# Performance work log

Measured on AMD Instinct MI355X. Metric: run time of the kernel, lower is better.

Reference implementation:

```python
import jax, jax.numpy as jnp
import numpy as np

H, C = 4, 32            # heads, per-head out channels -> H*C = 128
NEG = jnp.float32(-1e9) # stand-in for -inf mask (keeps grads finite)
NUM_LOC = 15            # self.num_locations hardcoded to 15


def _tconv(x, src, dst, ea, Wq, bq, Wk, bk, Wv, bv, We, Ws, bs, Wb):
    # PyG TransformerConv(beta=True, concat=True, edge_dim=1)
    N = x.shape[0]
    q = (x @ Wq + bq).reshape(N, H, C)
    k = (x @ Wk + bk).reshape(N, H, C)
    v = (x @ Wv + bv).reshape(N, H, C)
    e = (ea @ We).reshape(-1, H, C)  # edge embedding [E,H,C]
    kj = k[src] + e
    alpha = jnp.einsum('ehc,ehc->eh', q[dst], kj) / jnp.sqrt(jnp.float32(C))
    # scatter-softmax over incoming edges of each dst node
    amax = jax.ops.segment_max(alpha, dst, num_segments=N)
    ex = jnp.exp(alpha - amax[dst])
    den = jax.ops.segment_sum(ex, dst, num_segments=N)
    w = ex / (den[dst] + 1e-16)
    out = jax.ops.segment_sum((v[src] + e) * w[..., None], dst, num_segments=N).reshape(N, H * C)
    xr = x @ Ws + bs  # lin_skip
    beta = jax.nn.sigmoid(jnp.concatenate([out, xr, out - xr], axis=-1) @ Wb)  # [N,1]
    return beta * xr + (1.0 - beta) * out


def _bn(x, g, b):
    # BatchNorm1d in training mode (batch statistics, biased var)
    m = x.mean(0)
    v = ((x - m) ** 2).mean(0)
    return (x - m) * jax.lax.rsqrt(v + 1e-5) * g + b


def _forward_core(fa, edge_index, active_mask):
    (node_type, requests, latency,
     c0_Wq, c0_bq, c0_Wk, c0_bk, c0_Wv, c0_bv, c0_We, c0_Ws, c0_bs, c0_Wb,
     t0_W, t0_b, bn0_g, bn0_b,
     cs_Wq, cs_bq, cs_Wk, cs_bk, cs_Wv, cs_bv, cs_We, cs_Ws, cs_bs, cs_Wb,
     ts_W, ts_b, bns_g, bns_b,
     emb_W1, emb_b1, emb_W2, emb_b2, emb_W3, emb_b3,
     rem_W, rem_b, add_W, add_b) = fa
    src, dst = edge_index[0], edge_index[1]
    ea = latency[:, None]                      # edge_attr [E,1]
    x = jnp.stack([node_type, requests], axis=1)  # [N,2]
    # NetworkGraphEmbeddingConstructor: conv1 + 4 stacked conv/linear/bn blocks
    x = _tconv(x, src, dst, ea, c0_Wq, c0_bq, c0_Wk, c0_bk, c0_Wv, c0_bv, c0_We, c0_Ws, c0_bs, c0_Wb)
    x = _bn(jax.nn.relu(x @ t0_W + t0_b), bn0_g, bn0_b)
    for i in range(4):
        x = _tconv(x, src, dst, ea, cs_Wq[i], cs_bq[i], cs_Wk[i], cs_bk[i], cs_Wv[i], cs_bv[i], cs_We[i], cs_Ws[i], cs_bs[i], cs_Wb[i])
        x = _bn(jax.nn.relu(x @ ts_W[i] + ts_b[i]), bns_g[i], bns_b[i])
    # embedding_transformation MLP
    x = jax.nn.relu(x @ emb_W1 + emb_b1)
    x = jax.nn.relu(x @ emb_W2 + emb_b2)
    x = x @ emb_W3 + emb_b3                    # [N,64]
    # sampling head (batch_index=None branch)
    N = x.shape[0]
    maskf = jnp.where(active_mask == 1, jnp.float32(0.0), NEG)
    loc = jnp.arange(N) < NUM_LOC
    remove_mask = jnp.where(loc, jnp.where(maskf == 0.0, NEG, jnp.float32(0.0)), maskf)
    logits1 = (x @ rem_W + rem_b)[:, 0] + remove_mask
    k1, k2 = jax.random.split(jax.random.key(42))
    a1 = jnp.argmax(logits1 + jax.random.gumbel(k1, (N,), logits1.dtype))  # Categorical sample
    mask2 = maskf.at[a1].set(0.0)
    t = jnp.tanh(x[a1] @ add_W + add_b)        # [64]
    logits2 = x @ t + mask2
    a2 = jnp.argmax(logits2 + jax.random.gumbel(k2, (N,), logits2.dtype))
    log_probs = jnp.stack([jax.nn.log_softmax(logits1)[a1], jax.nn.log_softmax(logits2)[a2]])
    return jnp.stack([logits1, logits2]), jnp.stack([a1, a2]), log_probs


def setup_inputs() -> dict:
    N, E = 50000, 400000
    F, HC, EMB, L = 2, 128, 32, 4
    key = jax.random.key(0)
    kit = iter(jax.random.split(key, 64))
    def w(shape, s=0.1):
        return jax.random.normal(next(kit), shape, jnp.float32) * s
    return {
        'node_type': w((N,), 1.0),
        'requests': jax.random.uniform(next(kit), (N,), jnp.float32),
        'latency': jax.random.uniform(next(kit), (E,), jnp.float32),
        'edge_index': jax.random.randint(next(kit), (2, E), 0, N, jnp.int32),
        'active_mask': jax.random.randint(next(kit), (N,), 0, 2, jnp.int32),
        'c0_Wq': w((F, HC)), 'c0_bq': w((HC,)),
        'c0_Wk': w((F, HC)), 'c0_bk': w((HC,)),
        'c0_Wv': w((F, HC)), 'c0_bv': w((HC,)),
        'c0_We': w((1, HC)),
        'c0_Ws': w((F, HC)), 'c0_bs': w((HC,)),
        'c0_Wb': w((3 * HC, 1)),
        't0_W': w((HC, EMB)), 't0_b': w((EMB,)),
        'bn0_g': jnp.ones((EMB,), jnp.float32), 'bn0_b': jnp.zeros((EMB,), jnp.float32),
        'cs_Wq': w((L, EMB, HC)), 'cs_bq': w((L, HC)),
        'cs_Wk': w((L, EMB, HC)), 'cs_bk': w((L, HC)),
        'cs_Wv': w((L, EMB, HC)), 'cs_bv': w((L, HC)),
        'cs_We': w((L, 1, HC)),
        'cs_Ws': w((L, EMB, HC)), 'cs_bs': w((L, HC)),
        'cs_Wb': w((L, 3 * HC, 1)),
        'ts_W': w((L, HC, EMB)), 'ts_b': w((L, EMB)),
        'bns_g': jnp.ones((L, EMB), jnp.float32), 'bns_b': jnp.zeros((L, EMB), jnp.float32),
        'emb_W1': w((EMB, 128)), 'emb_b1': w((128,)),
        'emb_W2': w((128, 64)), 'emb_b2': w((64,)),
        'emb_W3': w((64, 64)), 'emb_b3': w((64,)),
        'rem_W': w((64, 1)), 'rem_b': w((1,)),
        'add_W': w((64, 64)), 'add_b': w((64,)),
    }


def reference(node_type, requests, latency, edge_index, active_mask,
              c0_Wq, c0_bq, c0_Wk, c0_bk, c0_Wv, c0_bv, c0_We, c0_Ws, c0_bs, c0_Wb,
              t0_W, t0_b, bn0_g, bn0_b,
              cs_Wq, cs_bq, cs_Wk, cs_bk, cs_Wv, cs_bv, cs_We, cs_Ws, cs_bs, cs_Wb,
              ts_W, ts_b, bns_g, bns_b,
              emb_W1, emb_b1, emb_W2, emb_b2, emb_W3, emb_b3,
              rem_W, rem_b, add_W, add_b):
    fa = (node_type, requests, latency,
          c0_Wq, c0_bq, c0_Wk, c0_bk, c0_Wv, c0_bv, c0_We, c0_Ws, c0_bs, c0_Wb,
          t0_W, t0_b, bn0_g, bn0_b,
          cs_Wq, cs_bq, cs_Wk, cs_bk, cs_Wv, cs_bv, cs_We, cs_Ws, cs_bs, cs_Wb,
          ts_W, ts_b, bns_g, bns_b,
          emb_W1, emb_b1, emb_W2, emb_b2, emb_W3, emb_b3,
          rem_W, rem_b, add_W, add_b)
    return _forward_core(fa, edge_index, active_mask)
```

## Files before the change

kernel.cpp:

```cpp
#include <hip/hip_runtime.h>
#include <hip/hip_fp16.h>
#include <cstdint>
#include <math.h>

typedef _Float16 h2 __attribute__((ext_vector_type(2)));

__device__ __forceinline__ h2 f2h2(float a, float b) {
    h2 r; r.x = (_Float16)a; r.y = (_Float16)b; return r;
}
__device__ __forceinline__ float fdot2f(h2 a, h2 b, float c) {
    return __builtin_amdgcn_fdot2(a, b, c, false);
}

union f4h {
    float4 f;
    h2 h[4];
    __half2 u[4];
};

__device__ __forceinline__ uint32_t rotl32(uint32_t x, uint32_t n) {
    return (x << n) | (x >> (32u - n));
}

__device__ __forceinline__ void tf2x32(uint32_t k0, uint32_t k1,
                                       uint32_t x0, uint32_t x1,
                                       uint32_t& o0, uint32_t& o1) {
    uint32_t k2 = k0 ^ k1 ^ 0x1BD11BDAu;
    x0 += k0; x1 += k1;
    x0 += x1; x1 = rotl32(x1, 13); x1 ^= x0;
    x0 += x1; x1 = rotl32(x1, 15); x1 ^= x0;
    x0 += x1; x1 = rotl32(x1, 26); x1 ^= x0;
    x0 += x1; x1 = rotl32(x1, 6);  x1 ^= x0;
    x0 += k1; x1 += k2 + 1u;
    x0 += x1; x1 = rotl32(x1, 17); x1 ^= x0;
    x0 += x1; x1 = rotl32(x1, 29); x1 ^= x0;
    x0 += x1; x1 = rotl32(x1, 16); x1 ^= x0;
    x0 += x1; x1 = rotl32(x1, 24); x1 ^= x0;
    x0 += k2; x1 += k0 + 2u;
    x0 += x1; x1 = rotl32(x1, 13); x1 ^= x0;
    x0 += x1; x1 = rotl32(x1, 15); x1 ^= x0;
    x0 += x1; x1 = rotl32(x1, 26); x1 ^= x0;
    x0 += x1; x1 = rotl32(x1, 6);  x1 ^= x0;
    x0 += k0; x1 += k1 + 3u;
    x0 += x1; x1 = rotl32(x1, 17); x1 ^= x0;
    x0 += x1; x1 = rotl32(x1, 29); x1 ^= x0;
    x0 += x1; x1 = rotl32(x1, 16); x1 ^= x0;
    x0 += x1; x1 = rotl32(x1, 24); x1 ^= x0;
    x0 += k1; x1 += k2 + 4u;
    x0 += x1; x1 = rotl32(x1, 13); x1 ^= x0;
    x0 += x1; x1 = rotl32(x1, 15); x1 ^= x0;
    x0 += x1; x1 = rotl32(x1, 26); x1 ^= x0;
    x0 += x1; x1 = rotl32(x1, 6);  x1 ^= x0;
    x0 += k2; x1 += k0 + 5u;
    o0 = x0; o1 = x1;
}

__device__ float gumbel_at(int n, int which, int N) {
    uint32_t a0, a1, b0, b1;
    tf2x32(0u, 42u, 0u, 2u, a0, a1);
    tf2x32(0u, 42u, 1u, 3u, b0, b1);
    uint32_t gk0 = which ? a1 : a0;
    uint32_t gk1 = which ? b1 : b0;
    int half = N >> 1;
    uint32_t o0, o1, bits;
    if (n < half) { tf2x32(gk0, gk1, (uint32_t)n, (uint32_t)(n + half), o0, o1); bits = o0; }
    else          { tf2x32(gk0, gk1, (uint32_t)(n - half), (uint32_t)n, o0, o1); bits = o1; }
    float f = __uint_as_float((bits >> 9) | 0x3F800000u) - 1.0f;
    float u = fmaxf(1.17549435e-38f, f);
    return -logf(-logf(u));
}

__device__ __forceinline__ uint32_t fmono(float f) {
    uint32_t b = __float_as_uint(f);
    return (b & 0x80000000u) ? ~b : (b | 0x80000000u);
}
__device__ __forceinline__ float funmono(uint32_t u) {
    uint32_t b = (u & 0x80000000u) ? (u & 0x7FFFFFFFu) : ~u;
    return __uint_as_float(b);
}

#define NEGF (-1e9f)
#define ATTNGRID 2048

__global__ void k_hist(const int* __restrict__ dstp, int* __restrict__ deg, int E) {
    int e = blockIdx.x * 256 + threadIdx.x;
    if (e < E) atomicAdd(&deg[dstp[e]], 1);
}

__global__ void k_scan1(const int* __restrict__ deg, int* __restrict__ bsum, int N) {
    __shared__ int s[256];
    int i = blockIdx.x * 256 + threadIdx.x;
    s[threadIdx.x] = (i < N) ? deg[i] : 0;
    __syncthreads();
    for (int st = 128; st > 0; st >>= 1) {
        if (threadIdx.x < st) s[threadIdx.x] += s[threadIdx.x + st];
        __syncthreads();
    }
    if (threadIdx.x == 0) bsum[blockIdx.x] = s[0];
}

__global__ void k_scan2(int* __restrict__ bsum, int nb) {
    __shared__ int s[256];
    int i = threadIdx.x;
    int v = (i < nb) ? bsum[i] : 0;
    s[i] = v;
    __syncthreads();
    for (int st = 1; st < 256; st <<= 1) {
        int t = (i >= st) ? s[i - st] : 0;
        __syncthreads();
        s[i] += t;
        __syncthreads();
    }
    if (i < nb) bsum[i] = s[i] - v;
}

__global__ void k_scan3(const int* __restrict__ deg, const int* __restrict__ bsum,
                        int* __restrict__ rowptr, int* __restrict__ cursor, int N) {
    __shared__ int s[256];
    int i = blockIdx.x * 256 + threadIdx.x;
    int v = (i < N) ? deg[i] : 0;
    s[threadIdx.x] = v;
    __syncthreads();
    for (int st = 1; st < 256; st <<= 1) {
        int t = (threadIdx.x >= st) ? s[threadIdx.x - st] : 0;
        __syncthreads();
        s[threadIdx.x] += t;
        __syncthreads();
    }
    int excl = s[threadIdx.x] - v + bsum[blockIdx.x];
    if (i < N) { rowptr[i] = excl; cursor[i] = excl; }
}

__global__ void k_fill(const int* __restrict__ dstp, const int* __restrict__ srcp,
                       const float* __restrict__ lat, int* __restrict__ cursor,
                       int2* __restrict__ srclat, int E) {
    int e = blockIdx.x * 256 + threadIdx.x;
    if (e < E) {
        int pos = atomicAdd(&cursor[dstp[e]], 1);
        srclat[pos] = make_int2(srcp[e], __float_as_int(lat[e]));
    }
}

__global__ __launch_bounds__(512, 4) void k_qkvr(
        const float* __restrict__ xin, const float* __restrict__ nt,
        const float* __restrict__ rq, int din, int N,
        const float* __restrict__ Wq, const float* __restrict__ bq,
        const float* __restrict__ Wk, const float* __restrict__ bk,
        const float* __restrict__ Wv, const float* __restrict__ bv,
        const float* __restrict__ Ws, const float* __restrict__ bs,
        const double* __restrict__ SUM, const double* __restrict__ SUMSQ,
        const float* __restrict__ bng, const float* __restrict__ bnb,
        int applyBN,
        __half* __restrict__ Q, __half* __restrict__ KV, __half* __restrict__ R) {
    __shared__ h2 w2[4][16 * 128];
    __shared__ float bias[4][128];
    __shared__ h2 xs2[32][17];
    __shared__ float sscale[32], sshift[32];
    int t = threadIdx.x;
    int dpCount = din >> 1;
    for (int i = t; i < dpCount * 128; i += 512) {
        int dp = i >> 7, j = i & 127;
        w2[0][i] = f2h2(Wq[(size_t)(2 * dp) * 128 + j], Wq[(size_t)(2 * dp + 1) * 128 + j]);
        w2[1][i] = f2h2(Wk[(size_t)(2 * dp) * 128 + j], Wk[(size_t)(2 * dp + 1) * 128 + j]);
        w2[2][i] = f2h2(Wv[(size_t)(2 * dp) * 128 + j], Wv[(size_t)(2 * dp + 1) * 128 + j]);
        w2[3][i] = f2h2(Ws[(size_t)(2 * dp) * 128 + j], Ws[(size_t)(2 * dp + 1) * 128 + j]);
    }
    if (t < 128) {
        bias[0][t] = bq[t]; bias[1][t] = bk[t]; bias[2][t] = bv[t]; bias[3][t] = bs[t];
    }
    if (t < 32) {
        if (applyBN) {
            double m = SUM[t] / N;
            double v = SUMSQ[t] / N - m * m;
            float inv = rsqrtf((float)v + 1e-5f);
            float sc = inv * bng[t];
            sscale[t] = sc;
            sshift[t] = bnb[t] - (float)m * sc;
        } else {
            sscale[t] = 1.f; sshift[t] = 0.f;
        }
    }
    int quad = t & 31;
    int sub = t >> 5;
    int dpsh = (din == 32) ? 4 : 0;
    int tiles = (N + 31) >> 5;
    for (int tile = blockIdx.x; tile < tiles; tile += gridDim.x) {
        int base = tile << 5;
        __syncthreads();
        for (int i = t; i < 32 * dpCount; i += 512) {
            int nl = i >> dpsh, dp = i & (dpCount - 1);
            int nn = base + nl;
            float x0 = 0.f, x1 = 0.f;
            if (nn < N) {
                if (din == 2) { x0 = nt[nn]; x1 = rq[nn]; }
                else {
                    x0 = xin[(size_t)nn * din + 2 * dp];
                    x1 = xin[(size_t)nn * din + 2 * dp + 1];
                }
            }
            x0 = x0 * sscale[2 * dp] + sshift[2 * dp];
            x1 = x1 * sscale[2 * dp + 1] + sshift[2 * dp + 1];
            xs2[nl][dp] = f2h2(x0, x1);
        }
        __syncthreads();
        float acc[4][2][4];
#pragma unroll
        for (int m = 0; m < 4; ++m)
#pragma unroll
            for (int k = 0; k < 2; ++k)
#pragma unroll
                for (int c = 0; c < 4; ++c) acc[m][k][c] = bias[m][quad * 4 + c];
        for (int dp = 0; dp < dpCount; ++dp) {
            h2 xv0 = xs2[sub * 2 + 0][dp];
            h2 xv1 = xs2[sub * 2 + 1][dp];
#pragma unroll
            for (int m = 0; m < 4; ++m) {
                const h2* wp = &w2[m][dp * 128 + quad * 4];
                h2 wa = wp[0], wb = wp[1], wc = wp[2], wd = wp[3];
                acc[m][0][0] = fdot2f(xv0, wa, acc[m][0][0]);
                acc[m][0][1] = fdot2f(xv0, wb, acc[m][0][1]);
                acc[m][0][2] = fdot2f(xv0, wc, acc[m][0][2]);
                acc[m][0][3] = fdot2f(xv0, wd, acc[m][0][3]);
                acc[m][1][0] = fdot2f(xv1, wa, acc[m][1][0]);
                acc[m][1][1] = fdot2f(xv1, wb, acc[m][1][1]);
                acc[m][1][2] = fdot2f(xv1, wc, acc[m][1][2]);
                acc[m][1][3] = fdot2f(xv1, wd, acc[m][1][3]);
            }
        }
#pragma unroll
        for (int k = 0; k < 2; ++k) {
            int n = base + sub * 2 + k;
            if (n < N) {
                *(__half2*)&Q[(size_t)n * 128 + quad * 4 + 0] =
                    __floats2half2_rn(acc[0][k][0], acc[0][k][1]);
                *(__half2*)&Q[(size_t)n * 128 + quad * 4 + 2] =
                    __floats2half2_rn(acc[0][k][2], acc[0][k][3]);
                *(__half2*)&KV[(size_t)n * 256 + quad * 4 + 0] =
                    __floats2half2_rn(acc[1][k][0], acc[1][k][1]);
                *(__half2*)&KV[(size_t)n * 256 + quad * 4 + 2] =
                    __floats2half2_rn(acc[1][k][2], acc[1][k][3]);
                *(__half2*)&KV[(size_t)n * 256 + 128 + quad * 4 + 0] =
                    __floats2half2_rn(acc[2][k][0], acc[2][k][1]);
                *(__half2*)&KV[(size_t)n * 256 + 128 + quad * 4 + 2] =
                    __floats2half2_rn(acc[2][k][2], acc[2][k][3]);
                *(__half2*)&R[(size_t)n * 128 + quad * 4 + 0] =
                    __floats2half2_rn(acc[3][k][0], acc[3][k][1]);
                *(__half2*)&R[(size_t)n * 128 + quad * 4 + 2] =
                    __floats2half2_rn(acc[3][k][2], acc[3][k][3]);
            }
        }
    }
}

__global__ __launch_bounds__(256) void k_attn(
        const int2* __restrict__ srclat,
        const __half* __restrict__ Q, const __half* __restrict__ KV,
        const float* __restrict__ We,
        const __half* __restrict__ R, const float* __restrict__ Wb,
        const int* __restrict__ rowptr, const int* __restrict__ deg,
        __half* __restrict__ A, int N) {
    int t = threadIdx.x;
    int wvid = t >> 6;
    int l64 = t & 63;
    int slot = l64 >> 4;
    int lane = l64 & 15;
    const float4 we4a = *(const float4*)&We[lane * 8 + 0];
    const float4 we4b = *(const float4*)&We[lane * 8 + 4];
    h2 weh0 = f2h2(we4a.x, we4a.y), weh1 = f2h2(we4a.z, we4a.w);
    h2 weh2 = f2h2(we4b.x, we4b.y), weh3 = f2h2(we4b.z, we4b.w);
    const float4 wb0a = *(const float4*)&Wb[lane * 8 + 0];
    const float4 wb0b = *(const float4*)&Wb[lane * 8 + 4];
    const float4 wb1a = *(const float4*)&Wb[128 + lane * 8 + 0];
    const float4 wb1b = *(const float4*)&Wb[128 + lane * 8 + 4];
    const float4 wb2a = *(const float4*)&Wb[256 + lane * 8 + 0];
    const float4 wb2b = *(const float4*)&Wb[256 + lane * 8 + 4];
    const float4 f4z = make_float4(0.f, 0.f, 0.f, 0.f);

    int waveGlobal = blockIdx.x * 4 + wvid;
    int totalWaves = gridDim.x * 4;

    f4h pq, pr;
    pq.f = f4z; pr.f = f4z;
    int pstart = 0, pd = 0;
    if (waveGlobal < N) {
        pq.f = *(const float4*)(Q + (size_t)waveGlobal * 128 + lane * 8);
        pr.f = *(const float4*)(R + (size_t)waveGlobal * 128 + lane * 8);
        pstart = rowptr[waveGlobal];
        pd = deg[waveGlobal];
    }

    for (int n = waveGlobal; n < N; n += totalWaves) {
        f4h qh = pq, rh = pr;
        int start = pstart, d = pd;

        int nn = n + totalWaves;
        if (nn < N) {
            pq.f = *(const float4*)(Q + (size_t)nn * 128 + lane * 8);
            pr.f = *(const float4*)(R + (size_t)nn * 128 + lane * 8);
            pstart = rowptr[nn];
            pd = deg[nn];
        }

        float qwe = fdot2f(qh.h[0], weh0, fdot2f(qh.h[1], weh1,
                    fdot2f(qh.h[2], weh2, fdot2f(qh.h[3], weh3, 0.f))));
        qwe += __shfl_xor(qwe, 1); qwe += __shfl_xor(qwe, 2);

        float m = -INFINITY, den = 0.f, plsum = 0.f;
        float a0 = 0.f, a1 = 0.f, a2 = 0.f, a3 = 0.f;
        float a4 = 0.f, a5 = 0.f, a6 = 0.f, a7 = 0.f;

        int idx = slot;
        bool have = idx < d;
        float l0 = 0.f;
        f4h k0, v0;
        k0.f = f4z; v0.f = f4z;
        if (have) {
            int2 sl = srclat[start + idx];
            l0 = __int_as_float(sl.y);
            k0.f = *(const float4*)(KV + (size_t)sl.x * 256 + lane * 8);
            v0.f = *(const float4*)(KV + (size_t)sl.x * 256 + 128 + lane * 8);
        }
        while (have) {
            int idx2 = idx + 4;
            bool have2 = idx2 < d;
            float l1 = 0.f;
            f4h k1, v1;
            k1.f = f4z; v1.f = f4z;
            if (have2) {
                int2 sl = srclat[start + idx2];
                l1 = __int_as_float(sl.y);
                k1.f = *(const float4*)(KV + (size_t)sl.x * 256 + lane * 8);
                v1.f = *(const float4*)(KV + (size_t)sl.x * 256 + 128 + lane * 8);
            }

            float t0 = fdot2f(qh.h[0], k0.h[0], fdot2f(qh.h[1], k0.h[1],
                       fdot2f(qh.h[2], k0.h[2], fdot2f(qh.h[3], k0.h[3], 0.f))));
            t0 += __shfl_xor(t0, 1); t0 += __shfl_xor(t0, 2);
            float alpha = fmaf(l0, qwe, t0) * 0.17677669529663687f;

            float mn = fmaxf(m, alpha);
            float sc = __expf(m - mn);
            float p = __expf(alpha - mn);
            a0 = a0 * sc + p * (float)v0.h[0].x;
            a1 = a1 * sc + p * (float)v0.h[0].y;
            a2 = a2 * sc + p * (float)v0.h[1].x;
            a3 = a3 * sc + p * (float)v0.h[1].y;
            a4 = a4 * sc + p * (float)v0.h[2].x;
            a5 = a5 * sc + p * (float)v0.h[2].y;
            a6 = a6 * sc + p * (float)v0.h[3].x;
            a7 = a7 * sc + p * (float)v0.h[3].y;
            plsum = plsum * sc + p * l0;
            den = den * sc + p;
            m = mn;

            idx = idx2; l0 = l1;
            k0.f = k1.f; v0.f = v1.f;
            have = have2;
        }

#pragma unroll
        for (int off = 16; off <= 32; off <<= 1) {
            float mo = __shfl_xor(m, off);
            float mn = fmaxf(m, mo);
            float sc = (m == -INFINITY) ? 0.f : __expf(m - mn);
            a0 *= sc; a1 *= sc; a2 *= sc; a3 *= sc;
            a4 *= sc; a5 *= sc; a6 *= sc; a7 *= sc;
            den *= sc; plsum *= sc;
            a0 += __shfl_xor(a0, off); a1 += __shfl_xor(a1, off);
            a2 += __shfl_xor(a2, off); a3 += __shfl_xor(a3, off);
            a4 += __shfl_xor(a4, off); a5 += __shfl_xor(a5, off);
            a6 += __shfl_xor(a6, off); a7 += __shfl_xor(a7, off);
            den += __shfl_xor(den, off); plsum += __shfl_xor(plsum, off);
            m = mn;
        }

        float inv = 1.f / (den + 1e-16f);
        float o0 = fmaf(plsum, we4a.x, a0) * inv;
        float o1 = fmaf(plsum, we4a.y, a1) * inv;
        float o2 = fmaf(plsum, we4a.z, a2) * inv;
        float o3 = fmaf(plsum, we4a.w, a3) * inv;
        float o4 = fmaf(plsum, we4b.x, a4) * inv;
        float o5 = fmaf(plsum, we4b.y, a5) * inv;
        float o6 = fmaf(plsum, we4b.z, a6) * inv;
        float o7 = fmaf(plsum, we4b.w, a7) * inv;

        float2 ra = __half22float2(rh.u[0]);
        float2 rb = __half22float2(rh.u[1]);
        float2 rc = __half22float2(rh.u[2]);
        float2 rd = __half22float2(rh.u[3]);
        float g = o0 * wb0a.x + ra.x * wb1a.x + (o0 - ra.x) * wb2a.x
                + o1 * wb0a.y + ra.y * wb1a.y + (o1 - ra.y) * wb2a.y
                + o2 * wb0a.z + rb.x * wb1a.z + (o2 - rb.x) * wb2a.z
                + o3 * wb0a.w + rb.y * wb1a.w + (o3 - rb.y) * wb2a.w
                + o4 * wb0b.x + rc.x * wb1b.x + (o4 - rc.x) * wb2b.x
                + o5 * wb0b.y + rc.y * wb1b.y + (o5 - rc.y) * wb2b.y
                + o6 * wb0b.z + rd.x * wb1b.z + (o6 - rd.x) * wb2b.z
                + o7 * wb0b.w + rd.y * wb1b.w + (o7 - rd.y) * wb2b.w;
        g += __shfl_xor(g, 1); g += __shfl_xor(g, 2);
        g += __shfl_xor(g, 4); g += __shfl_xor(g, 8);
        float beta = 1.0f / (1.0f + __expf(-g));

        if (slot == 0) {
            float b1 = 1.0f - beta;
            *(__half2*)&A[(size_t)n * 128 + lane * 8 + 0] =
                __floats2half2_rn(beta * ra.x + b1 * o0, beta * ra.y + b1 * o1);
            *(__half2*)&A[(size_t)n * 128 + lane * 8 + 2] =
                __floats2half2_rn(beta * rb.x + b1 * o2, beta * rb.y + b1 * o3);
            *(__half2*)&A[(size_t)n * 128 + lane * 8 + 4] =
                __floats2half2_rn(beta * rc.x + b1 * o4, beta * rc.y + b1 * o5);
            *(__half2*)&A[(size_t)n * 128 + lane * 8 + 6] =
                __floats2half2_rn(beta * rd.x + b1 * o6, beta * rd.y + b1 * o7);
        }
    }
}

__global__ __launch_bounds__(256) void k_linstats(
        const __half* __restrict__ A, const float* __restrict__ tW,
        const float* __restrict__ tb, float* __restrict__ H32,
        double* __restrict__ partials, int N) {
    __shared__ h2 w2l[64 * 32];
    __shared__ float bias[32];
    __shared__ h2 xsT[64][66];
    __shared__ double sp1[4][8][4], sp2[4][8][4];
    int t = threadIdx.x;
    for (int i = t; i < 64 * 32; i += 256) {
        int dp = i >> 5, j = i & 31;
        w2l[i] = f2h2(tW[(size_t)(2 * dp) * 32 + j], tW[(size_t)(2 * dp + 1) * 32 + j]);
    }
    if (t < 32) bias[t] = tb[t];
    int quad = t & 7;
    int sub = t >> 3;
    int base = blockIdx.x << 6;

    __syncthreads();
#pragma unroll
    for (int k = 0; k < 4; ++k) {
        int i = t + 256 * k;
        int nl = i >> 4, g8 = i & 15;
        int n = base + nl;
        h2 hv[4];
        if (n < N) {
            const h2* ap = (const h2*)(A + (size_t)n * 128 + g8 * 8);
            hv[0] = ap[0]; hv[1] = ap[1]; hv[2] = ap[2]; hv[3] = ap[3];
        } else {
            h2 z; z.x = (_Float16)0.f; z.y = (_Float16)0.f;
            hv[0] = z; hv[1] = z; hv[2] = z; hv[3] = z;
        }
        xsT[g8 * 4 + 0][nl] = hv[0];
        xsT[g8 * 4 + 1][nl] = hv[1];
        xsT[g8 * 4 + 2][nl] = hv[2];
        xsT[g8 * 4 + 3][nl] = hv[3];
    }
    __syncthreads();

    float acc[2][4];
#pragma unroll
    for (int k = 0; k < 2; ++k)
#pragma unroll
        for (int c = 0; c < 4; ++c) acc[k][c] = bias[quad * 4 + c];
    for (int dp = 0; dp < 64; ++dp) {
        h2 x0 = xsT[dp][sub * 2 + 0];
        h2 x1 = xsT[dp][sub * 2 + 1];
        const h2* wp = &w2l[dp * 32 + quad * 4];
        h2 wa = wp[0], wb = wp[1], wc = wp[2], wd = wp[3];
        acc[0][0] = fdot2f(x0, wa, acc[0][0]);
        acc[0][1] = fdot2f(x0, wb, acc[0][1]);
        acc[0][2] = fdot2f(x0, wc, acc[0][2]);
        acc[0][3] = fdot2f(x0, wd, acc[0][3]);
        acc[1][0] = fdot2f(x1, wa, acc[1][0]);
        acc[1][1] = fdot2f(x1, wb, acc[1][1]);
        acc[1][2] = fdot2f(x1, wc, acc[1][2]);
        acc[1][3] = fdot2f(x1, wd, acc[1][3]);
    }
    double s1[4] = {0, 0, 0, 0}, s2[4] = {0, 0, 0, 0};
#pragma unroll
    for (int k = 0; k < 2; ++k) {
        int n = base + sub * 2 + k;
        if (n < N) {
            float4 yv;
            yv.x = fmaxf(acc[k][0], 0.f); yv.y = fmaxf(acc[k][1], 0.f);
            yv.z = fmaxf(acc[k][2], 0.f); yv.w = fmaxf(acc[k][3], 0.f);
            *(float4*)&H32[(size_t)n * 32 + quad * 4] = yv;
            s1[0] += yv.x; s1[1] += yv.y; s1[2] += yv.z; s1[3] += yv.w;
            s2[0] += (double)yv.x * yv.x; s2[1] += (double)yv.y * yv.y;
            s2[2] += (double)yv.z * yv.z; s2[3] += (double)yv.w * yv.w;
        }
    }
#pragma unroll
    for (int c = 0; c < 4; ++c) {
        s1[c] += __shfl_xor(s1[c], 8);  s2[c] += __shfl_xor(s2[c], 8);
        s1[c] += __shfl_xor(s1[c], 16); s2[c] += __shfl_xor(s2[c], 16);
        s1[c] += __shfl_xor(s1[c], 32); s2[c] += __shfl_xor(s2[c], 32);
    }
    __syncthreads();
    int wave = t >> 6;
    if ((t & 63) < 8) {
#pragma unroll
        for (int c = 0; c < 4; ++c) { sp1[wave][quad][c] = s1[c]; sp2[wave][quad][c] = s2[c]; }
    }
    __syncthreads();
    if (t < 32) {
        int q = t >> 2, c = t & 3;
        double a1 = 0, a2 = 0;
#pragma unroll
        for (int wv = 0; wv < 4; ++wv) { a1 += sp1[wv][q][c]; a2 += sp2[wv][q][c]; }
        partials[(size_t)blockIdx.x * 64 + t] = a1;
        partials[(size_t)blockIdx.x * 64 + 32 + t] = a2;
    }
}

__global__ void k_statred(const double* __restrict__ partials,
                          double* __restrict__ SUM, double* __restrict__ SUMSQ,
                          int nblocks) {
    __shared__ double s[256];
    int col = blockIdx.x;
    double a = 0;
    for (int b = threadIdx.x; b < nblocks; b += 256)
        a += partials[(size_t)b * 64 + col];
    s[threadIdx.x] = a;
    __syncthreads();
    for (int st = 128; st > 0; st >>= 1) {
        if (threadIdx.x < st) s[threadIdx.x] += s[threadIdx.x + st];
        __syncthreads();
    }
    if (threadIdx.x == 0) {
        if (col < 32) SUM[col] = s[0];
        else SUMSQ[col - 32] = s[0];
    }
}

__global__ __launch_bounds__(256) void k_mlp1(
        const float* __restrict__ H32,
        const double* __restrict__ SUM, const double* __restrict__ SUMSQ,
        const float* __restrict__ bng, const float* __restrict__ bnb,
        const float* __restrict__ W1, const float* __restrict__ b1,
        float* __restrict__ Y1, unsigned int* __restrict__ smallbuf, int N) {
    __shared__ float w1[32 * 128];
    __shared__ float sb1[128];
    __shared__ float sscale[32], sshift[32];
    __shared__ float xs[32][36];
    int t = threadIdx.x;
    if (blockIdx.x == 0 && t < 16) smallbuf[t] = 0u;
    for (int i = t; i < 32 * 128; i += 256) w1[i] = W1[i];
    if (t < 128) sb1[t] = b1[t];
    if (t < 32) {
        double m = SUM[t] / N;
        double v = SUMSQ[t] / N - m * m;
        float inv = rsqrtf((float)v + 1e-5f);
        float sc = inv * bng[t];
        sscale[t] = sc;
        sshift[t] = bnb[t] - (float)m * sc;
    }
    int quad = t & 31, sub = t >> 5;
    int tiles = (N + 31) >> 5;
    for (int tile = blockIdx.x; tile < tiles; tile += gridDim.x) {
        int base = tile << 5;
        __syncthreads();
        {
            int nl = t >> 3, q = t & 7;
            int n = base + nl;
            float4 xv = make_float4(0.f, 0.f, 0.f, 0.f);
            if (n < N) xv = *(const float4*)&H32[(size_t)n * 32 + q * 4];
            xs[nl][q * 4 + 0] = xv.x * sscale[q * 4 + 0] + sshift[q * 4 + 0];
            xs[nl][q * 4 + 1] = xv.y * sscale[q * 4 + 1] + sshift[q * 4 + 1];
            xs[nl][q * 4 + 2] = xv.z * sscale[q * 4 + 2] + sshift[q * 4 + 2];
            xs[nl][q * 4 + 3] = xv.w * sscale[q * 4 + 3] + sshift[q * 4 + 3];
        }
        __syncthreads();
        float a[4][4];
#pragma unroll
        for (int k = 0; k < 4; ++k)
#pragma unroll
            for (int c = 0; c < 4; ++c) a[k][c] = sb1[quad * 4 + c];
        for (int d = 0; d < 32; ++d) {
            float4 w4 = *(const float4*)&w1[d * 128 + quad * 4];
#pragma unroll
            for (int k = 0; k < 4; ++k) {
                float x = xs[sub * 4 + k][d];
                a[k][0] = fmaf(x, w4.x, a[k][0]);
                a[k][1] = fmaf(x, w4.y, a[k][1]);
                a[k][2] = fmaf(x, w4.z, a[k][2]);
                a[k][3] = fmaf(x, w4.w, a[k][3]);
            }
        }
#pragma unroll
        for (int k = 0; k < 4; ++k) {
            int n = base + sub * 4 + k;
            if (n < N) {
                float4 yv;
                yv.x = fmaxf(a[k][0], 0.f); yv.y = fmaxf(a[k][1], 0.f);
                yv.z = fmaxf(a[k][2], 0.f); yv.w = fmaxf(a[k][3], 0.f);
                *(float4*)&Y1[(size_t)n * 128 + quad * 4] = yv;
            }
        }
    }
}

__global__ __launch_bounds__(256) void k_mlp2(
        const float* __restrict__ Y1, const float* __restrict__ W2,
        const float* __restrict__ b2, float* __restrict__ Y2, int N) {
    __shared__ float w2f[128 * 64];
    __shared__ float sb2[64];
    __shared__ float xs[32][132];
    int t = threadIdx.x;
    for (int i = t; i < 128 * 64; i += 256) w2f[i] = W2[i];
    if (t < 64) sb2[t] = b2[t];
    int quad = t & 15, sub = t >> 4;
    int tiles = (N + 31) >> 5;
    for (int tile = blockIdx.x; tile < tiles; tile += gridDim.x) {
        int base = tile << 5;
        __syncthreads();
#pragma unroll
        for (int k = 0; k < 4; ++k) {
            int i = t + 256 * k;
            int nl = i >> 5, q = i & 31;
            int n = base + nl;
            float4 xv = make_float4(0.f, 0.f, 0.f, 0.f);
            if (n < N) xv = *(const float4*)&Y1[(size_t)n * 128 + q * 4];
            *(float4*)&xs[nl][q * 4] = xv;
        }
        __syncthreads();
        float a[2][4];
#pragma unroll
        for (int k = 0; k < 2; ++k)
#pragma unroll
            for (int c = 0; c < 4; ++c) a[k][c] = sb2[quad * 4 + c];
        for (int d = 0; d < 128; ++d) {
            float4 w4 = *(const float4*)&w2f[d * 64 + quad * 4];
#pragma unroll
            for (int k = 0; k < 2; ++k) {
                float x = xs[sub * 2 + k][d];
                a[k][0] = fmaf(x, w4.x, a[k][0]);
                a[k][1] = fmaf(x, w4.y, a[k][1]);
                a[k][2] = fmaf(x, w4.z, a[k][2]);
                a[k][3] = fmaf(x, w4.w, a[k][3]);
            }
        }
#pragma unroll
        for (int k = 0; k < 2; ++k) {
            int n = base + sub * 2 + k;
            if (n < N) {
                float4 yv;
                yv.x = fmaxf(a[k][0], 0.f); yv.y = fmaxf(a[k][1], 0.f);
                yv.z = fmaxf(a[k][2], 0.f); yv.w = fmaxf(a[k][3], 0.f);
                *(float4*)&Y2[(size_t)n * 64 + quad * 4] = yv;
            }
        }
    }
}

__global__ __launch_bounds__(256) void k_mlp3(
        const float* __restrict__ Y2, const float* __restrict__ W3,
        const float* __restrict__ b3, float* __restrict__ X3, int N) {
    __shared__ float w3[64 * 64];
    __shared__ float sb3[64];
    __shared__ float xs[32][68];
    int t = threadIdx.x;
    for (int i = t; i < 64 * 64; i += 256) w3[i] = W3[i];
    if (t < 64) sb3[t] = b3[t];
    int quad = t & 15, sub = t >> 4;
    int tiles = (N + 31) >> 5;
    for (int tile = blockIdx.x; tile < tiles; tile += gridDim.x) {
        int base = tile << 5;
        __syncthreads();
#pragma unroll
        for (int k = 0; k < 2; ++k) {
            int i = t + 256 * k;
            int nl = i >> 4, q = i & 15;
            int n = base + nl;
            float4 xv = make_float4(0.f, 0.f, 0.f, 0.f);
            if (n < N) xv = *(const float4*)&Y2[(size_t)n * 64 + q * 4];
            *(float4*)&xs[nl][q * 4] = xv;
        }
        __syncthreads();
        float a[2][4];
#pragma unroll
        for (int k = 0; k < 2; ++k)
#pragma unroll
            for (int c = 0; c < 4; ++c) a[k][c] = sb3[quad * 4 + c];
        for (int d = 0; d < 64; ++d) {
            float4 w4 = *(const float4*)&w3[d * 64 + quad * 4];
#pragma unroll
            for (int k = 0; k < 2; ++k) {
                float x = xs[sub * 2 + k][d];
                a[k][0] = fmaf(x, w4.x, a[k][0]);
                a[k][1] = fmaf(x, w4.y, a[k][1]);
                a[k][2] = fmaf(x, w4.z, a[k][2]);
                a[k][3] = fmaf(x, w4.w, a[k][3]);
            }
        }
#pragma unroll
        for (int k = 0; k < 2; ++k) {
            int n = base + sub * 2 + k;
            if (n < N)
                *(float4*)&X3[(size_t)n * 64 + quad * 4] = *(float4*)a[k];
        }
    }
}

__global__ void k_head1(const float* __restrict__ X3, const float* __restrict__ remW,
                        const float* __restrict__ remB, const int* __restrict__ active,
                        float* __restrict__ l1out, unsigned long long* __restrict__ slot1,
                        unsigned int* __restrict__ m1, int N) {
    int n = blockIdx.x * 256 + threadIdx.x;
    if (n >= N) return;
    const float* xr = X3 + (size_t)n * 64;
    float acc = remB[0];
    for (int d = 0; d < 64; d++) acc = fmaf(xr[d], remW[d], acc);
    float maskf = (active[n] == 1) ? 0.f : NEGF;
    float rm = (n < 15) ? ((maskf == 0.f) ? NEGF : 0.f) : maskf;
    float l1 = acc + rm;
    l1out[n] = l1;
    atomicMax(m1, fmono(l1));
    float z = l1 + gumbel_at(n, 0, N);
    unsigned long long p = ((unsigned long long)fmono(z) << 32) |
                           (unsigned long long)(0xFFFFFFFFu - (unsigned)n);
    atomicMax(slot1, p);
}

__global__ void k_head2(const float* __restrict__ X3, const float* __restrict__ addW,
                        const float* __restrict__ addB,
                        const unsigned long long* __restrict__ slot1,
                        float* __restrict__ tvec, int* __restrict__ a1buf) {
    int j = threadIdx.x;
    unsigned long long p = *slot1;
    int a1 = (int)(0xFFFFFFFFu - (unsigned)(p & 0xFFFFFFFFull));
    const float* xr = X3 + (size_t)a1 * 64;
    float acc = addB[j];
    for (int d = 0; d < 64; d++) acc = fmaf(xr[d], addW[d * 64 + j], acc);
    tvec[j] = tanhf(acc);
    if (j == 0) *a1buf = a1;
}

__global__ void k_head3(const float* __restrict__ X3, const float* __restrict__ tvec,
                        const int* __restrict__ active, const int* __restrict__ a1buf,
                        float* __restrict__ l2out, unsigned long long* __restrict__ slot2,
                        unsigned int* __restrict__ m2, int N) {
    int n = blockIdx.x * 256 + threadIdx.x;
    if (n >= N) return;
    const float* xr = X3 + (size_t)n * 64;
    float acc = 0.f;
    for (int d = 0; d < 64; d++) acc = fmaf(xr[d], tvec[d], acc);
    float maskf = (active[n] == 1) ? 0.f : NEGF;
    if (n == *a1buf) maskf = 0.f;
    float l2 = acc + maskf;
    l2out[n] = l2;
    atomicMax(m2, fmono(l2));
    float z = l2 + gumbel_at(n, 1, N);
    unsigned long long p = ((unsigned long long)fmono(z) << 32) |
                           (unsigned long long)(0xFFFFFFFFu - (unsigned)n);
    atomicMax(slot2, p);
}

__global__ void k_sumexp(const float* __restrict__ l1, const float* __restrict__ l2,
                         const unsigned int* __restrict__ m1, const unsigned int* __restrict__ m2,
                         float* __restrict__ se, int N) {
    int t = blockIdx.x * 256 + threadIdx.x;
    float M1 = funmono(*m1), M2 = funmono(*m2);
    float e1 = 0.f, e2 = 0.f;
    if (t < N) { e1 = expf(l1[t] - M1); e2 = expf(l2[t] - M2); }
    __shared__ float r1[256], r2[256];
    r1[threadIdx.x] = e1; r2[threadIdx.x] = e2;
    __syncthreads();
    for (int s = 128; s > 0; s >>= 1) {
        if (threadIdx.x < s) { r1[threadIdx.x] += r1[threadIdx.x + s]; r2[threadIdx.x] += r2[threadIdx.x + s]; }
        __syncthreads();
    }
    if (threadIdx.x == 0) { atomicAdd(&se[0], r1[0]); atomicAdd(&se[1], r2[0]); }
}

__global__ void k_final(const float* __restrict__ l1, const float* __restrict__ l2,
                        const unsigned long long* __restrict__ slot2,
                        const int* __restrict__ a1buf,
                        const unsigned int* __restrict__ m1, const unsigned int* __restrict__ m2,
                        const float* __restrict__ se, float* __restrict__ outTail, int N) {
    int a1 = *a1buf;
    int a2 = (int)(0xFFFFFFFFu - (unsigned)((*slot2) & 0xFFFFFFFFull));
    outTail[0] = (float)a1;
    outTail[1] = (float)a2;
    outTail[2] = l1[a1] - (funmono(*m1) + logf(se[0]));
    outTail[3] = l2[a2] - (funmono(*m2) + logf(se[1]));
}

extern "C" void kernel_launch(void* const* d_in, const int* in_sizes, int n_in,
                              void* d_out, int out_size, void* d_ws, size_t ws_size,
                              hipStream_t stream) {
    const float* node_type = (const float*)d_in[0];
    const float* requests  = (const float*)d_in[1];
    const float* latency   = (const float*)d_in[2];
    const int* edge_index  = (const int*)d_in[3];
    const int* active      = (const int*)d_in[4];
    int N = in_sizes[0];
    int E = in_sizes[2];
    const int* src = edge_index;
    const int* dst = edge_index + E;
    float* out = (float*)d_out;

    char* base = (char*)d_ws;
    size_t off = 0;
    auto alloc = [&](size_t bytes) -> char* {
        char* p = base + off;
        off += (bytes + 255) & ~(size_t)255;
        return p;
    };
    char* Abuf   = alloc((size_t)N * 128 * 4);
    char* Qbuf   = alloc((size_t)N * 128 * 4);
    __half* KV   = (__half*)alloc((size_t)N * 256 * 2);
    char* Rbuf   = alloc((size_t)N * 128 * 4);
    float* H32   = (float*)alloc((size_t)N * 32 * 4);
    int* deg     = (int*)alloc((size_t)N * 4);
    int* rowptr  = (int*)alloc((size_t)N * 4);
    int* cursor  = (int*)alloc((size_t)N * 4);
    int2* srclat = (int2*)alloc((size_t)E * 8);
    int* bsum    = (int*)alloc(1024 * 4);
    int lsTiles = (N + 63) / 64;
    double* partials = (double*)alloc((size_t)lsTiles * 64 * 8);
    double* SUM  = (double*)alloc(512);
    double* SUMSQ = SUM + 32;
    char* small  = alloc(1024);
    unsigned long long* slot1 = (unsigned long long*)small;
    unsigned long long* slot2 = slot1 + 1;
    unsigned int* m1 = (unsigned int*)(small + 16);
    unsigned int* m2 = m1 + 1;
    float* se = (float*)(small + 24);
    int* a1buf = (int*)(small + 32);
    float* tvec = (float*)(small + 64);

    __half* Ah = (__half*)Abuf;   float* Y2f = (float*)Abuf;
    __half* Qh = (__half*)Qbuf;   float* Y1f = (float*)Qbuf;
    __half* Rh = (__half*)Rbuf;   float* X3f = (float*)Rbuf;

    int ng = (N + 255) / 256;
    int egE = (E + 255) / 256;
    int nb = ng;

    (void)hipMemsetAsync(deg, 0, (size_t)N * 4, stream);
    k_hist<<<egE, 256, 0, stream>>>(dst, deg, E);
    k_scan1<<<nb, 256, 0, stream>>>(deg, bsum, N);
    k_scan2<<<1, 256, 0, stream>>>(bsum, nb);
    k_scan3<<<nb, 256, 0, stream>>>(deg, bsum, rowptr, cursor, N);
    k_fill<<<egE, 256, 0, stream>>>(dst, src, latency, cursor, srclat, E);

    for (int L = 0; L < 5; ++L) {
        int din = L ? 32 : 2;
        const float* xin = L ? H32 : nullptr;
        const float* Wq = L ? (const float*)d_in[19] + (size_t)(L - 1) * 4096 : (const float*)d_in[5];
        const float* bq = L ? (const float*)d_in[20] + (size_t)(L - 1) * 128  : (const float*)d_in[6];
        const float* Wk = L ? (const float*)d_in[21] + (size_t)(L - 1) * 4096 : (const float*)d_in[7];
        const float* bk = L ? (const float*)d_in[22] + (size_t)(L - 1) * 128  : (const float*)d_in[8];
        const float* Wv = L ? (const float*)d_in[23] + (size_t)(L - 1) * 4096 : (const float*)d_in[9];
        const float* bv = L ? (const float*)d_in[24] + (size_t)(L - 1) * 128  : (const float*)d_in[10];
        const float* We = L ? (const float*)d_in[25] + (size_t)(L - 1) * 128  : (const float*)d_in[11];
        const float* Ws = L ? (const float*)d_in[26] + (size_t)(L - 1) * 4096 : (const float*)d_in[12];
        const float* bs = L ? (const float*)d_in[27] + (size_t)(L - 1) * 128  : (const float*)d_in[13];
        const float* Wb = L ? (const float*)d_in[28] + (size_t)(L - 1) * 384  : (const float*)d_in[14];
        const float* tW = L ? (const float*)d_in[29] + (size_t)(L - 1) * 4096 : (const float*)d_in[15];
        const float* tb = L ? (const float*)d_in[30] + (size_t)(L - 1) * 32   : (const float*)d_in[16];
        const float* bngP = (L == 1) ? (const float*)d_in[17]
                          : (L >= 2) ? (const float*)d_in[31] + (size_t)(L - 2) * 32 : nullptr;
        const float* bnbP = (L == 1) ? (const float*)d_in[18]
                          : (L >= 2) ? (const float*)d_in[32] + (size_t)(L - 2) * 32 : nullptr;

        k_qkvr<<<1024, 512, 0, stream>>>(xin, node_type, requests, din, N,
                                         Wq, bq, Wk, bk, Wv, bv, Ws, bs,
                                         SUM, SUMSQ, bngP, bnbP, (L > 0) ? 1 : 0,
                                         Qh, KV, Rh);
        k_attn<<<ATTNGRID, 256, 0, stream>>>(srclat, Qh, KV, We, Rh, Wb,
                                             rowptr, deg, Ah, N);
        k_linstats<<<lsTiles, 256, 0, stream>>>(Ah, tW, tb, H32, partials, N);
        k_statred<<<64, 256, 0, stream>>>(partials, SUM, SUMSQ, lsTiles);
    }

    k_mlp1<<<512, 256, 0, stream>>>(H32, SUM, SUMSQ,
                                    (const float*)d_in[31] + 3 * 32,
                                    (const float*)d_in[32] + 3 * 32,
                                    (const float*)d_in[33], (const float*)d_in[34],
                                    Y1f, (unsigned int*)small, N);
    k_mlp2<<<512, 256, 0, stream>>>(Y1f, (const float*)d_in[35], (const float*)d_in[36],
                                    Y2f, N);
    k_mlp3<<<512, 256, 0, stream>>>(Y2f, (const float*)d_in[37], (const float*)d_in[38],
                                    X3f, N);
    k_head1<<<ng, 256, 0, stream>>>(X3f, (const float*)d_in[39], (const float*)d_in[40],
                                    active, out, slot1, m1, N);
    k_head2<<<1, 64, 0, stream>>>(X3f, (const float*)d_in[41], (const float*)d_in[42],
                                  slot1, tvec, a1buf);
    k_head3<<<ng, 256, 0, stream>>>(X3f, tvec, active, a1buf, out + N, slot2, m2, N);
    k_sumexp<<<ng, 256, 0, stream>>>(out, out + N, m1, m2, se, N);
    k_final<<<1, 1, 0, stream>>>(out, out + N, slot2, a1buf, m1, m2, se, out + 2 * N, N);
}
```

Baseline: 734.6 us.

## Fuse post-attention linear, ReLU and batch-stat partials into attention kernel

Moves the 128->32 linear layer, ReLU and the per-column sum and sum-of-squares accumulation into the attention kernel. Each wave stages its combined output row in shared memory and computes the 32 outputs with packed fp16 dot products. This drops the fp16 intermediate buffer A and the separate k_linstats launch, saving one global write and read of N*128 halves per layer. In exchange, each attention block must first stage the transposed weight matrix in shared memory, and every node now pays extra per-wave dot-product work plus shuffles.

```diff
diff --git a/kernel.cpp b/kernel.cpp
--- a/kernel.cpp
+++ b/kernel.cpp
@@ -258,8 +258,24 @@
         const float* __restrict__ We,
         const __half* __restrict__ R, const float* __restrict__ Wb,
         const int* __restrict__ rowptr, const int* __restrict__ deg,
-        __half* __restrict__ A, int N) {
+        const float* __restrict__ tW, const float* __restrict__ tb,
+        float* __restrict__ H32, double* __restrict__ partials, int N) {
+    __shared__ f4h tw4[32 * 17];
+    __shared__ float tbias[32];
+    __shared__ f4h aLDS[4][16];
+    __shared__ double sp1[4][32], sp2[4][32];
     int t = threadIdx.x;
+    {
+        h2* tw2 = (h2*)tw4;
+        for (int i = t; i < 32 * 64; i += 256) {
+            int j = i >> 6, dp = i & 63;
+            tw2[j * 68 + dp] = f2h2(tW[(size_t)(2 * dp) * 32 + j],
+                                    tW[(size_t)(2 * dp + 1) * 32 + j]);
+        }
+        if (t < 32) tbias[t] = tb[t];
+    }
+    __syncthreads();
+
     int wvid = t >> 6;
     int l64 = t & 63;
     int slot = l64 >> 4;
@@ -276,6 +292,10 @@
     const float4 wb2b = *(const float4*)&Wb[256 + lane * 8 + 4];
     const float4 f4z = make_float4(0.f, 0.f, 0.f, 0.f);
 
+    int col = l64 & 31;
+    int hh = l64 >> 5;
+    double s1 = 0.0, s2 = 0.0;
+
     int waveGlobal = blockIdx.x * 4 + wvid;
     int totalWaves = gridDim.x * 4;
 
@@ -402,110 +422,46 @@
 
         if (slot == 0) {
             float b1 = 1.0f - beta;
-            *(__half2*)&A[(size_t)n * 128 + lane * 8 + 0] =
-                __floats2half2_rn(beta * ra.x + b1 * o0, beta * ra.y + b1 * o1);
-            *(__half2*)&A[(size_t)n * 128 + lane * 8 + 2] =
-                __floats2half2_rn(beta * rb.x + b1 * o2, beta * rb.y + b1 * o3);
-            *(__half2*)&A[(size_t)n * 128 + lane * 8 + 4] =
-                __floats2half2_rn(beta * rc.x + b1 * o4, beta * rc.y + b1 * o5);
-            *(__half2*)&A[(size_t)n * 128 + lane * 8 + 6] =
-                __floats2half2_rn(beta * rd.x + b1 * o6, beta * rd.y + b1 * o7);
-        }
-    }
-}
-
-__global__ __launch_bounds__(256) void k_linstats(
-        const __half* __restrict__ A, const float* __restrict__ tW,
-        const float* __restrict__ tb, float* __restrict__ H32,
-        double* __restrict__ partials, int N) {
-    __shared__ h2 w2l[64 * 32];
-    __shared__ float bias[32];
-    __shared__ h2 xsT[64][66];
-    __shared__ double sp1[4][8][4], sp2[4][8][4];
-    int t = threadIdx.x;
-    for (int i = t; i < 64 * 32; i += 256) {
-        int dp = i >> 5, j = i & 31;
-        w2l[i] = f2h2(tW[(size_t)(2 * dp) * 32 + j], tW[(size_t)(2 * dp + 1) * 32 + j]);
-    }
-    if (t < 32) bias[t] = tb[t];
-    int quad = t & 7;
-    int sub = t >> 3;
-    int base = blockIdx.x << 6;
+            f4h av;
+            av.u[0] = __floats2half2_rn(beta * ra.x + b1 * o0, beta * ra.y + b1 * o1);
+            av.u[1] = __floats2half2_rn(beta * rb.x + b1 * o2, beta * rb.y + b1 * o3);
+            av.u[2] = __floats2half2_rn(beta * rc.x + b1 * o4, beta * rc.y + b1 * o5);
+            av.u[3] = __floats2half2_rn(beta * rd.x + b1 * o6, beta * rd.y + b1 * o7);
+            aLDS[wvid][lane].f = av.f;
+        }
+        {
+            const f4h* ap = &aLDS[wvid][hh * 8];
+            const f4h* twf = &tw4[col * 17 + hh * 8];
+            float accv = 0.f;
+#pragma unroll
+            for (int i = 0; i < 8; ++i) {
+                f4h aw, ww;
+                aw.f = ap[i].f;
+                ww.f = twf[i].f;
+                accv = fdot2f(aw.h[0], ww.h[0], accv);
+                accv = fdot2f(aw.h[1], ww.h[1], accv);
+                accv = fdot2f(aw.h[2], ww.h[2], accv);
+                accv = fdot2f(aw.h[3], ww.h[3], accv);
+            }
+            accv += __shfl_xor(accv, 32);
+            if (hh == 0) {
+                float y = fmaxf(accv + tbias[col], 0.f);
+                H32[(size_t)n * 32 + col] = y;
+                s1 += y;
+                s2 += (double)y * y;
+            }
+        }
+    }
 
     __syncthreads();
-#pragma unroll
-    for (int k = 0; k < 4; ++k) {
-        int i = t + 256 * k;
-        int nl = i >> 4, g8 = i & 15;
-        int n = base + nl;
-        h2 hv[4];
-        if (n < N) {
-            const h2* ap = (const h2*)(A + (size_t)n * 128 + g8 * 8);
-            hv[0] = ap[0]; hv[1] = ap[1]; hv[2] = ap[2]; hv[3] = ap[3];
-        } else {
-            h2 z; z.x = (_Float16)0.f; z.y = (_Float16)0.f;
-            hv[0] = z; hv[1] = z; hv[2] = z; hv[3] = z;
-        }
-        xsT[g8 * 4 + 0][nl] = hv[0];
-        xsT[g8 * 4 + 1][nl] = hv[1];
-        xsT[g8 * 4 + 2][nl] = hv[2];
-        xsT[g8 * 4 + 3][nl] = hv[3];
-    }
+    if (l64 < 32) { sp1[wvid][l64] = s1; sp2[wvid][l64] = s2; }
     __syncthreads();
-
-    float acc[2][4];
-#pragma unroll
-    for (int k = 0; k < 2; ++k)
-#pragma unroll
-        for (int c = 0; c < 4; ++c) acc[k][c] = bias[quad * 4 + c];
-    for (int dp = 0; dp < 64; ++dp) {
-        h2 x0 = xsT[dp][sub * 2 + 0];
-        h2 x1 = xsT[dp][sub * 2 + 1];
-        const h2* wp = &w2l[dp * 32 + quad * 4];
-        h2 wa = wp[0], wb = wp[1], wc = wp[2], wd = wp[3];
-        acc[0][0] = fdot2f(x0, wa, acc[0][0]);
-        acc[0][1] = fdot2f(x0, wb, acc[0][1]);
-        acc[0][2] = fdot2f(x0, wc, acc[0][2]);
-        acc[0][3] = fdot2f(x0, wd, acc[0][3]);
-        acc[1][0] = fdot2f(x1, wa, acc[1][0]);
-        acc[1][1] = fdot2f(x1, wb, acc[1][1]);
-        acc[1][2] = fdot2f(x1, wc, acc[1][2]);
-        acc[1][3] = fdot2f(x1, wd, acc[1][3]);
-    }
-    double s1[4] = {0, 0, 0, 0}, s2[4] = {0, 0, 0, 0};
-#pragma unroll
-    for (int k = 0; k < 2; ++k) {
-        int n = base + sub * 2 + k;
-        if (n < N) {
-            float4 yv;
-            yv.x = fmaxf(acc[k][0], 0.f); yv.y = fmaxf(acc[k][1], 0.f);
-            yv.z = fmaxf(acc[k][2], 0.f); yv.w = fmaxf(acc[k][3], 0.f);
-            *(float4*)&H32[(size_t)n * 32 + quad * 4] = yv;
-            s1[0] += yv.x; s1[1] += yv.y; s1[2] += yv.z; s1[3] += yv.w;
-            s2[0] += (double)yv.x * yv.x; s2[1] += (double)yv.y * yv.y;
-            s2[2] += (double)yv.z * yv.z; s2[3] += (double)yv.w * yv.w;
-        }
-    }
-#pragma unroll
-    for (int c = 0; c < 4; ++c) {
-        s1[c] += __shfl_xor(s1[c], 8);  s2[c] += __shfl_xor(s2[c], 8);
-        s1[c] += __shfl_xor(s1[c], 16); s2[c] += __shfl_xor(s2[c], 16);
-        s1[c] += __shfl_xor(s1[c], 32); s2[c] += __shfl_xor(s2[c], 32);
-    }
-    __syncthreads();
-    int wave = t >> 6;
-    if ((t & 63) < 8) {
-#pragma unroll
-        for (int c = 0; c < 4; ++c) { sp1[wave][quad][c] = s1[c]; sp2[wave][quad][c] = s2[c]; }
-    }
-    __syncthreads();
-    if (t < 32) {
-        int q = t >> 2, c = t & 3;
-        double a1 = 0, a2 = 0;
-#pragma unroll
-        for (int wv = 0; wv < 4; ++wv) { a1 += sp1[wv][q][c]; a2 += sp2[wv][q][c]; }
-        partials[(size_t)blockIdx.x * 64 + t] = a1;
-        partials[(size_t)blockIdx.x * 64 + 32 + t] = a2;
+    if (t < 64) {
+        int c = t & 31, which = t >> 5;
+        double a = 0.0;
+#pragma unroll
+        for (int w = 0; w < 4; ++w) a += which ? sp2[w][c] : sp1[w][c];
+        partials[(size_t)blockIdx.x * 64 + which * 32 + c] = a;
     }
 }
 
@@ -813,8 +769,7 @@
     int* cursor  = (int*)alloc((size_t)N * 4);
     int2* srclat = (int2*)alloc((size_t)E * 8);
     int* bsum    = (int*)alloc(1024 * 4);
-    int lsTiles = (N + 63) / 64;
-    double* partials = (double*)alloc((size_t)lsTiles * 64 * 8);
+    double* partials = (double*)alloc((size_t)ATTNGRID * 64 * 8);
     double* SUM  = (double*)alloc(512);
     double* SUMSQ = SUM + 32;
     char* small  = alloc(1024);
@@ -826,7 +781,7 @@
     int* a1buf = (int*)(small + 32);
     float* tvec = (float*)(small + 64);
 
-    __half* Ah = (__half*)Abuf;   float* Y2f = (float*)Abuf;
+    float* Y2f = (float*)Abuf;
     __half* Qh = (__half*)Qbuf;   float* Y1f = (float*)Qbuf;
     __half* Rh = (__half*)Rbuf;   float* X3f = (float*)Rbuf;
 
@@ -866,9 +821,9 @@
                                          SUM, SUMSQ, bngP, bnbP, (L > 0) ? 1 : 0,
                                          Qh, KV, Rh);
         k_attn<<<ATTNGRID, 256, 0, stream>>>(srclat, Qh, KV, We, Rh, Wb,
-                                             rowptr, deg, Ah, N);
-        k_linstats<<<lsTiles, 256, 0, stream>>>(Ah, tW, tb, H32, partials, N);
-        k_statred<<<64, 256, 0, stream>>>(partials, SUM, SUMSQ, lsTiles);
+                                             rowptr, deg, tW, tb,
+                                             H32, partials, N);
+        k_statred<<<64, 256, 0, stream>>>(partials, SUM, SUMSQ, ATTNGRID);
     }
 
     k_mlp1<<<512, 256, 0, stream>>>(H32, SUM, SUMSQ,
```

Result: slower. 820.5 us (+11.7%).

## Deepen software prefetch pipeline across nodes in attention aggregation kernel

Applied to the files above, without the earlier changes.

Extends the per-wave node loop's prefetching from one stage to three. Row pointers and degrees are fetched three nodes ahead, the first edge's src/latency record two nodes ahead, and the next node's Q, R and first K/V rows one node ahead. The goal is to hide the dependent-load latency chain (rowptr, then srclat, then KV) behind the current node's computation. In exchange it holds more live registers, which could lower occupancy.

```diff
diff --git a/kernel.cpp b/kernel.cpp
--- a/kernel.cpp
+++ b/kernel.cpp
@@ -276,29 +276,53 @@
     const float4 wb2b = *(const float4*)&Wb[256 + lane * 8 + 4];
     const float4 f4z = make_float4(0.f, 0.f, 0.f, 0.f);
 
-    int waveGlobal = blockIdx.x * 4 + wvid;
-    int totalWaves = gridDim.x * 4;
-
-    f4h pq, pr;
-    pq.f = f4z; pr.f = f4z;
-    int pstart = 0, pd = 0;
-    if (waveGlobal < N) {
-        pq.f = *(const float4*)(Q + (size_t)waveGlobal * 128 + lane * 8);
-        pr.f = *(const float4*)(R + (size_t)waveGlobal * 128 + lane * 8);
-        pstart = rowptr[waveGlobal];
-        pd = deg[waveGlobal];
-    }
-
-    for (int n = waveGlobal; n < N; n += totalWaves) {
-        f4h qh = pq, rh = pr;
-        int start = pstart, d = pd;
-
-        int nn = n + totalWaves;
-        if (nn < N) {
-            pq.f = *(const float4*)(Q + (size_t)nn * 128 + lane * 8);
-            pr.f = *(const float4*)(R + (size_t)nn * 128 + lane * 8);
-            pstart = rowptr[nn];
-            pd = deg[nn];
+    int T = gridDim.x * 4;
+    int n0 = blockIdx.x * 4 + wvid;
+
+    f4h qh, rh, k0, v0;
+    int start = 0, d = 0; float l0 = 0.f;
+    f4h pq, pr, pk, pv;
+    float pl = 0.f;
+    int s1 = 0, d1 = 0;
+    int2 psl1 = make_int2(0, 0);
+    int s2 = 0, d2 = 0;
+    qh.f = f4z; rh.f = f4z; k0.f = f4z; v0.f = f4z;
+    pq.f = f4z; pr.f = f4z; pk.f = f4z; pv.f = f4z;
+
+    if (n0 < N) {
+        start = rowptr[n0]; d = deg[n0];
+        qh.f = *(const float4*)(Q + (size_t)n0 * 128 + lane * 8);
+        rh.f = *(const float4*)(R + (size_t)n0 * 128 + lane * 8);
+        if (slot < d) {
+            int2 sl = srclat[start + slot];
+            l0 = __int_as_float(sl.y);
+            k0.f = *(const float4*)(KV + (size_t)sl.x * 256 + lane * 8);
+            v0.f = *(const float4*)(KV + (size_t)sl.x * 256 + 128 + lane * 8);
+        }
+        int n1 = n0 + T;
+        if (n1 < N) {
+            s1 = rowptr[n1]; d1 = deg[n1];
+            if (slot < d1) psl1 = srclat[s1 + slot];
+        }
+        int n2 = n0 + 2 * T;
+        if (n2 < N) { s2 = rowptr[n2]; d2 = deg[n2]; }
+    }
+
+    for (int n = n0; n < N; n += T) {
+        int n1 = n + T, n2 = n + 2 * T, n3 = n + 3 * T;
+        int s3 = 0, d3 = 0;
+        if (n3 < N) { s3 = rowptr[n3]; d3 = deg[n3]; }
+        int2 psl2 = make_int2(0, 0);
+        if (n2 < N && slot < d2) psl2 = srclat[s2 + slot];
+        pq.f = f4z; pr.f = f4z; pk.f = f4z; pv.f = f4z; pl = 0.f;
+        if (n1 < N) {
+            pq.f = *(const float4*)(Q + (size_t)n1 * 128 + lane * 8);
+            pr.f = *(const float4*)(R + (size_t)n1 * 128 + lane * 8);
+            if (slot < d1) {
+                pl = __int_as_float(psl1.y);
+                pk.f = *(const float4*)(KV + (size_t)psl1.x * 256 + lane * 8);
+                pv.f = *(const float4*)(KV + (size_t)psl1.x * 256 + 128 + lane * 8);
+            }
         }
 
         float qwe = fdot2f(qh.h[0], weh0, fdot2f(qh.h[1], weh1,
@@ -311,15 +335,6 @@
 
         int idx = slot;
         bool have = idx < d;
-        float l0 = 0.f;
-        f4h k0, v0;
-        k0.f = f4z; v0.f = f4z;
-        if (have) {
-            int2 sl = srclat[start + idx];
-            l0 = __int_as_float(sl.y);
-            k0.f = *(const float4*)(KV + (size_t)sl.x * 256 + lane * 8);
-            v0.f = *(const float4*)(KV + (size_t)sl.x * 256 + 128 + lane * 8);
-        }
         while (have) {
             int idx2 = idx + 4;
             bool have2 = idx2 < d;
@@ -411,6 +426,11 @@
             *(__half2*)&A[(size_t)n * 128 + lane * 8 + 6] =
                 __floats2half2_rn(beta * rd.x + b1 * o6, beta * rd.y + b1 * o7);
         }
+
+        qh.f = pq.f; rh.f = pr.f; k0.f = pk.f; v0.f = pv.f; l0 = pl;
+        start = s1; d = d1;
+        s1 = s2; d1 = d2; s2 = s3; d2 = d3;
+        psl1 = psl2;
     }
 }
 
```

Measured after the change: 732.2 us. Within noise of the previous version (-0.3%).
